# Performance work log

Measured on AMD Instinct MI355X. Metric: run time of the kernel, lower is better.

The kernel has to match this reference:

```python
import jax, jax.numpy as jnp
import numpy as np
from jax import lax

VEHICLE_LABELS = jnp.array([2, 3, 4, 6, 8], dtype=jnp.int64)
IMNET_MEAN = jnp.array([0.485, 0.456, 0.406], dtype=jnp.float32)
IMNET_STD = jnp.array([0.229, 0.224, 0.225], dtype=jnp.float32)
CROP = 64  # fixed RoIAlign output resolution replacing the variable-size python crop loop


def setup_inputs() -> dict:
    key = jax.random.key(0)
    ks = jax.random.split(key, 8)
    B, N, H, W = 8, 300, 512, 512
    x = jax.random.uniform(ks[0], (B, 3, H, W), dtype=jnp.float32)
    # well-formed boxes [x_min, y_min, x_max, y_max] inside the image
    tl = jax.random.uniform(ks[1], (B, N, 2), dtype=jnp.float32) * (W - 64.0)
    wh = jax.random.uniform(ks[2], (B, N, 2), dtype=jnp.float32) * 192.0 + 16.0
    br = jnp.minimum(tl + wh, float(W))
    boxes = jnp.concatenate([tl, br], axis=-1)  # [B,N,4]
    scores = jax.random.uniform(ks[3], (B, N), dtype=jnp.float32)
    labels = jax.random.randint(ks[4], (B, N), 0, 91).astype(jnp.int64)
    Wc = jax.random.normal(ks[5], (256, 3, 7, 7), dtype=jnp.float32) * 0.1
    bc = jnp.zeros((256,), dtype=jnp.float32)
    Wf = jax.random.normal(ks[6], (256, 4096), dtype=jnp.float32) / np.sqrt(256.0)
    bf = jnp.zeros((4096,), dtype=jnp.float32)
    return {"x": x, "boxes": boxes, "scores": scores, "labels": labels,
            "Wc": Wc, "bc": bc, "Wf": Wf, "bf": bf}


def extractor(imgs, Wc, bc, Wf, bf):
    # imgs [N,3,h,w] -> [N,4096]
    y = lax.conv_general_dilated(imgs, Wc, (4, 4), 'SAME',
                                 dimension_numbers=('NCHW', 'OIHW', 'NCHW'))
    y = jax.nn.relu(y + bc[None, :, None, None])
    y = y.mean(axis=(2, 3))  # global average pool -> [N,256]
    return y @ Wf + bf


def bilinear_sample(img, ys, xs):
    # img [C,H,W], ys [S], xs [S] -> [C,S,S]
    C, H, W = img.shape
    y0f = jnp.floor(ys); x0f = jnp.floor(xs)
    wy = (ys - y0f)[None, :, None]
    wx = (xs - x0f)[None, None, :]
    y0 = jnp.clip(y0f.astype(jnp.int32), 0, H - 1); y1 = jnp.clip(y0 + 1, 0, H - 1)
    x0 = jnp.clip(x0f.astype(jnp.int32), 0, W - 1); x1 = jnp.clip(x0 + 1, 0, W - 1)
    Ia = img[:, y0][:, :, x0]; Ib = img[:, y0][:, :, x1]
    Ic = img[:, y1][:, :, x0]; Id = img[:, y1][:, :, x1]
    return (Ia * (1 - wy) * (1 - wx) + Ib * (1 - wy) * wx
            + Ic * wy * (1 - wx) + Id * wy * wx)


def roi_align(img, box):
    # img [C,H,W], box [4] = x_min,y_min,x_max,y_max -> [C,CROP,CROP]
    t = (jnp.arange(CROP, dtype=img.dtype) + 0.5) / CROP
    ys = box[1] + t * (box[3] - box[1])
    xs = box[0] + t * (box[2] - box[0])
    return bilinear_sample(img, ys, xs)


def reference(x, boxes, scores, labels, Wc, bc, Wf, bf):
    score_threshold, K = 0.8, 20
    B = x.shape[0]
    # detection-weights transforms: ImageNet normalization
    images = (x - IMNET_MEAN[None, :, None, None]) / IMNET_STD[None, :, None, None]
    fullframe_features = extractor(images, Wc, bc, Wf, bf)  # [B,4096]
    # vehicle-class + score-threshold filtering, then top-k selection
    class_mask = (labels[..., None] == VEHICLE_LABELS[None, None, :]).any(-1)  # [B,N]
    comb_mask = class_mask & (scores > score_threshold)
    masked_scores = jnp.where(comb_mask, scores, -jnp.inf)
    vals, idx = lax.top_k(masked_scores, K)  # [B,K]
    valid = vals > -jnp.inf  # True where there is an object (matches torch code: 1=object)
    sel = jnp.take_along_axis(boxes, idx[..., None], axis=1)  # [B,K,4]
    Objects = jnp.where(valid[..., None], sel, 0.0)  # [B,K,4]
    # fused batched crop (RoIAlign) + batched extractor, replacing per-object loop
    crops = jax.vmap(lambda im, bxs: jax.vmap(lambda b: roi_align(im, b))(bxs))(images, Objects)  # [B,K,3,CROP,CROP]
    feats = extractor(crops.reshape(B * K, 3, CROP, CROP), Wc, bc, Wf, bf).reshape(B, K, 4096)
    degenerate = (Objects[..., 2] <= Objects[..., 0]) | (Objects[..., 3] <= Objects[..., 1])
    Object_features = jnp.where((valid & ~degenerate)[..., None], feats, 0.0)  # [B,K,4096]
    return Objects, Object_features, valid, fullframe_features
```

## Files before the change

kernel.cpp:

```cpp
#include <hip/hip_runtime.h>
#include <hip/hip_bf16.h>

#define OBJ_OFF   0
#define FEAT_OFF  640
#define VALID_OFF 656000
#define FF_OFF    656160

#define POOLED_N  (168 * 256)
#define SELBOX_N  (160 * 4)
#define FLAGS_N   (160)
#define K3        192

typedef __attribute__((ext_vector_type(8))) short short8v;
typedef __attribute__((ext_vector_type(4))) short short4v;
typedef __attribute__((ext_vector_type(4))) float f32x4;

__device__ __forceinline__ unsigned int rne_bf16(float f) {
    unsigned int u = __float_as_uint(f);
    return (u + 0x7FFFu + ((u >> 16) & 1u)) >> 16;
}

__global__ __launch_bounds__(256) void prep_kernel(
    const float* __restrict__ Wc, unsigned short* __restrict__ Wb,
    float* __restrict__ pooled)
{
    int i = blockIdx.x * 256 + threadIdx.x;
    if (i < POOLED_N) pooled[i] = 0.f;
    int oc = i / K3, k = i % K3;
    int c = k >> 6, r = (k >> 3) & 7, q = k & 7;
    float v = (r < 7 && q < 7) ? Wc[oc * 147 + c * 49 + r * 7 + q] : 0.f;
    Wb[i] = (unsigned short)rne_bf16(v);
}

__global__ __launch_bounds__(512) void topk_kernel(
    const float* __restrict__ boxes, const float* __restrict__ scores,
    const int* __restrict__ labels, float* __restrict__ d_out,
    float* __restrict__ selbox, float* __restrict__ flags)
{
    __shared__ unsigned long long keys[512];
    __shared__ unsigned long long red[512];
    const int b = blockIdx.x, t = threadIdx.x;

    unsigned long long key = 0ULL;
    if (t < 300) {
        float s = scores[b * 300 + t];
        int   l = labels[b * 300 + t];
        bool cls = (l == 2) || (l == 3) || (l == 4) || (l == 6) || (l == 8);
        if (cls && s > 0.8f) {
            key = ((unsigned long long)__float_as_uint(s) << 32) |
                  (unsigned long long)(unsigned int)(~(unsigned int)t);
        }
    }
    keys[t] = key;
    __syncthreads();

    for (int k = 0; k < 20; ++k) {
        red[t] = keys[t];
        __syncthreads();
        for (int s = 256; s > 0; s >>= 1) {
            if (t < s) red[t] = (red[t] > red[t + s]) ? red[t] : red[t + s];
            __syncthreads();
        }
        unsigned long long m = red[0];
        const int slot = b * 20 + k;
        if (m == 0ULL) {
            if (t == 0) {
                d_out[OBJ_OFF + slot * 4 + 0] = 0.f;
                d_out[OBJ_OFF + slot * 4 + 1] = 0.f;
                d_out[OBJ_OFF + slot * 4 + 2] = 0.f;
                d_out[OBJ_OFF + slot * 4 + 3] = 0.f;
                d_out[VALID_OFF + slot] = 0.f;
                selbox[slot * 4 + 0] = 0.f; selbox[slot * 4 + 1] = 0.f;
                selbox[slot * 4 + 2] = 0.f; selbox[slot * 4 + 3] = 0.f;
                flags[slot] = 0.f;
            }
        } else if (keys[t] == m) {
            const float bx0 = boxes[(b * 300 + t) * 4 + 0];
            const float by0 = boxes[(b * 300 + t) * 4 + 1];
            const float bx1 = boxes[(b * 300 + t) * 4 + 2];
            const float by1 = boxes[(b * 300 + t) * 4 + 3];
            d_out[OBJ_OFF + slot * 4 + 0] = bx0;
            d_out[OBJ_OFF + slot * 4 + 1] = by0;
            d_out[OBJ_OFF + slot * 4 + 2] = bx1;
            d_out[OBJ_OFF + slot * 4 + 3] = by1;
            d_out[VALID_OFF + slot] = 1.f;
            selbox[slot * 4 + 0] = bx0; selbox[slot * 4 + 1] = by0;
            selbox[slot * 4 + 2] = bx1; selbox[slot * 4 + 3] = by1;
            bool deg = (bx1 <= bx0) || (by1 <= by0);
            flags[slot] = deg ? 0.f : 1.f;
            keys[t] = 0ULL;
        }
        __syncthreads();
    }
}

__device__ __forceinline__ void conv_compute_regB(
    const unsigned short (&tb)[3][20][68], const short8v (&breg)[6][4],
    const float (&bias)[4], float (&poolacc)[4], int lr, int lq)
{
    f32x4 acc[4][4];
#pragma unroll
    for (int mf = 0; mf < 4; ++mf)
#pragma unroll
        for (int nf = 0; nf < 4; ++nf)
            acc[mf][nf] = (f32x4){0.f, 0.f, 0.f, 0.f};

#pragma unroll
    for (int ks = 0; ks < 6; ++ks) {
        const int kq = ks * 4 + lq;
        const int c = kq >> 3, rr = kq & 7;
        short8v a[4];
#pragma unroll
        for (int mf = 0; mf < 4; ++mf) {
            const unsigned short* ap = &tb[c][mf * 4 + rr][lr * 4];
            short4v a0 = *(const short4v*)ap;
            short4v a1 = *(const short4v*)(ap + 4);
            a[mf] = __builtin_shufflevector(a0, a1, 0, 1, 2, 3, 4, 5, 6, 7);
        }
#pragma unroll
        for (int mf = 0; mf < 4; ++mf)
#pragma unroll
            for (int nf = 0; nf < 4; ++nf)
                acc[mf][nf] = __builtin_amdgcn_mfma_f32_16x16x32_bf16(
                    a[mf], breg[ks][nf], acc[mf][nf], 0, 0, 0);
    }

#pragma unroll
    for (int nf = 0; nf < 4; ++nf) {
        float s = 0.f;
#pragma unroll
        for (int mf = 0; mf < 4; ++mf)
#pragma unroll
            for (int r = 0; r < 4; ++r) {
                float pv = acc[mf][nf][r] + bias[nf];
                s += pv > 0.f ? pv : 0.f;
            }
        poolacc[nf] += s;
    }
}

__device__ __forceinline__ void ff_stage_issue(
    const float* __restrict__ img, int iy0, int ix0, int tid, float (&sv)[16])
{
#pragma unroll
    for (int it = 0; it < 16; ++it) {
        int i = tid + it * 256;
        float v = 0.f;
        if (i < 4080) {
            int c = i / 1360, rem = i % 1360;
            int ir = rem / 68, icol = rem % 68;
            int gy = iy0 + ir, gx = ix0 + icol;
            if (gy >= 0 && gy < 512 && gx >= 0 && gx < 512)
                v = img[((size_t)c * 512 + gy) * 512 + gx];
        }
        sv[it] = v;
    }
}

__device__ __forceinline__ void ff_stage_write(
    unsigned short (&tb)[3][20][68], int iy0, int ix0, int tid,
    const float (&sv)[16], const float* mean, const float* istd)
{
#pragma unroll
    for (int it = 0; it < 16; ++it) {
        int i = tid + it * 256;
        if (i < 4080) {
            int c = i / 1360, rem = i % 1360;
            int ir = rem / 68, icol = rem % 68;
            int gy = iy0 + ir, gx = ix0 + icol;
            bool inb = (gy >= 0 && gy < 512 && gx >= 0 && gx < 512);
            float nv = inb ? (sv[it] - mean[c]) * istd[c] : 0.f;
            ((unsigned short*)tb)[i] = (unsigned short)rne_bf16(nv);
        }
    }
}

__global__ __launch_bounds__(256, 2) void ffconv_mfma(
    const float* __restrict__ x, const unsigned short* __restrict__ Wb,
    const float* __restrict__ bc, float* __restrict__ pooled)
{
    __shared__ __align__(16) unsigned short buf[2][3][20][68];
    const int b = blockIdx.y;
    const int tile_x = blockIdx.x & 7, rblk = blockIdx.x >> 3;
    const int tid = threadIdx.x;
    const int w = tid >> 6, l = tid & 63, lr = l & 15, lq = l >> 4;
    const int n0 = w * 64;
    const int ix0 = tile_x * 64 - 1;

    const float mean[3] = {0.485f, 0.456f, 0.406f};
    const float istd[3] = {1.0f / 0.229f, 1.0f / 0.224f, 1.0f / 0.225f};
    const float* __restrict__ img = x + (size_t)b * 3 * 512 * 512;

    short8v breg[6][4];
#pragma unroll
    for (int ks = 0; ks < 6; ++ks)
#pragma unroll
        for (int nf = 0; nf < 4; ++nf)
            breg[ks][nf] = *(const short8v*)&Wb[(size_t)(n0 + nf * 16 + lr) * K3 + ks * 32 + lq * 8];

    float bias[4];
#pragma unroll
    for (int nf = 0; nf < 4; ++nf) bias[nf] = bc[n0 + nf * 16 + lr];

    float poolacc[4] = {0.f, 0.f, 0.f, 0.f};
    float sv[16];

    ff_stage_issue(img, (rblk * 4 + 0) * 16 - 1, ix0, tid, sv);
    ff_stage_write(buf[0], (rblk * 4 + 0) * 16 - 1, ix0, tid, sv, mean, istd);
    __syncthreads();

#pragma unroll
    for (int q = 0; q < 4; ++q) {
        const int cur = q & 1;
        if (q < 3) ff_stage_issue(img, (rblk * 4 + q + 1) * 16 - 1, ix0, tid, sv);
        conv_compute_regB(buf[cur], breg, bias, poolacc, lr, lq);
        if (q < 3)
            ff_stage_write(buf[cur ^ 1], (rblk * 4 + q + 1) * 16 - 1, ix0, tid, sv, mean, istd);
        __syncthreads();
    }

#pragma unroll
    for (int nf = 0; nf < 4; ++nf) {
        float s = poolacc[nf];
        s += __shfl_down(s, 32);
        s += __shfl_down(s, 16);
        if (l < 16) atomicAdd(&pooled[b * 256 + n0 + nf * 16 + lr], s);
    }
}

__device__ __forceinline__ void conv_core(
    const unsigned short (&tile)[3][20][68],
    const unsigned short* __restrict__ Wb, const float* __restrict__ bc,
    float* __restrict__ pooled, int prow, int tid)
{
    const int w = tid >> 6, l = tid & 63;
    const int lr = l & 15, lq = l >> 4;
    const int n0 = w * 64;

    f32x4 acc[4][4];
#pragma unroll
    for (int mf = 0; mf < 4; ++mf)
#pragma unroll
        for (int nf = 0; nf < 4; ++nf)
            acc[mf][nf] = (f32x4){0.f, 0.f, 0.f, 0.f};

#pragma unroll
    for (int ks = 0; ks < 6; ++ks) {
        const int kq = ks * 4 + lq;
        const int c = kq >> 3, rr = kq & 7;
        const int koff = ks * 32 + lq * 8;

        short8v a[4], bfr[4];
#pragma unroll
        for (int mf = 0; mf < 4; ++mf) {
            const unsigned short* ap = &tile[c][mf * 4 + rr][lr * 4];
            short4v a0 = *(const short4v*)ap;
            short4v a1 = *(const short4v*)(ap + 4);
            a[mf] = __builtin_shufflevector(a0, a1, 0, 1, 2, 3, 4, 5, 6, 7);
        }
#pragma unroll
        for (int nf = 0; nf < 4; ++nf)
            bfr[nf] = *(const short8v*)&Wb[(size_t)(n0 + nf * 16 + lr) * K3 + koff];
#pragma unroll
        for (int mf = 0; mf < 4; ++mf)
#pragma unroll
            for (int nf = 0; nf < 4; ++nf)
                acc[mf][nf] = __builtin_amdgcn_mfma_f32_16x16x32_bf16(
                    a[mf], bfr[nf], acc[mf][nf], 0, 0, 0);
    }

#pragma unroll
    for (int nf = 0; nf < 4; ++nf) {
        const int oc = n0 + nf * 16 + lr;
        const float bias = bc[oc];
        float s = 0.f;
#pragma unroll
        for (int mf = 0; mf < 4; ++mf)
#pragma unroll
            for (int r = 0; r < 4; ++r) {
                float pv = acc[mf][nf][r] + bias;
                s += pv > 0.f ? pv : 0.f;
            }
        s += __shfl_down(s, 32);
        s += __shfl_down(s, 16);
        if (l < 16) atomicAdd(&pooled[prow * 256 + oc], s);
    }
}

__global__ __launch_bounds__(256, 2) void cropconv_mfma(
    const float* __restrict__ x, const unsigned short* __restrict__ Wb,
    const float* __restrict__ bc, const float* __restrict__ selbox,
    const float* __restrict__ flags, float* __restrict__ pooled)
{
    const int bk = blockIdx.x >> 2, quarter = blockIdx.x & 3;
    if (flags[bk] == 0.f) return;
    const int b = bk / 20;
    const int tid = threadIdx.x;

    __shared__ __align__(16) unsigned short tile[3][20][68];

    const float bx0 = selbox[bk * 4 + 0], by0 = selbox[bk * 4 + 1];
    const float bx1 = selbox[bk * 4 + 2], by1 = selbox[bk * 4 + 3];
    const float sy = (by1 - by0) * (1.f / 64.f);
    const float sx = (bx1 - bx0) * (1.f / 64.f);

    const float mean[3] = {0.485f, 0.456f, 0.406f};
    const float istd[3] = {1.0f / 0.229f, 1.0f / 0.224f, 1.0f / 0.225f};
    const float* __restrict__ img = x + (size_t)b * 3 * 512 * 512;

#pragma unroll
    for (int rd = 0; rd < 2; ++rd) {
        float rva[8], rvb[8], rvc[8], rvd[8], rwy[8], rwx[8];
#pragma unroll
        for (int e = 0; e < 8; ++e) {
            int i = tid + (rd * 8 + e) * 256;
            float Ia = 0.f, Ib = 0.f, Ic = 0.f, Id = 0.f, wy = 0.f, wx = 0.f;
            if (i < 4080) {
                int c = i / 1360, rem = i % 1360;
                int ir = rem / 68, icol = rem % 68;
                int cy = quarter * 16 - 1 + ir, cx = icol - 1;
                if (cy >= 0 && cy < 64 && cx >= 0 && cx < 64) {
                    float ys = by0 + ((float)cy + 0.5f) * sy;
                    float xs = bx0 + ((float)cx + 0.5f) * sx;
                    float yf = floorf(ys), xf = floorf(xs);
                    wy = ys - yf; wx = xs - xf;
                    int iy0 = min(max((int)yf, 0), 511), iy1 = min(iy0 + 1, 511);
                    int ix0 = min(max((int)xf, 0), 511), ix1 = min(ix0 + 1, 511);
                    const float* ch = img + (size_t)c * 512 * 512;
                    Ia = ch[iy0 * 512 + ix0]; Ib = ch[iy0 * 512 + ix1];
                    Ic = ch[iy1 * 512 + ix0]; Id = ch[iy1 * 512 + ix1];
                }
            }
            rva[e] = Ia; rvb[e] = Ib; rvc[e] = Ic; rvd[e] = Id;
            rwy[e] = wy; rwx[e] = wx;
        }
#pragma unroll
        for (int e = 0; e < 8; ++e) {
            int i = tid + (rd * 8 + e) * 256;
            if (i < 4080) {
                int c = i / 1360, rem = i % 1360;
                int ir = rem / 68, icol = rem % 68;
                int cy = quarter * 16 - 1 + ir, cx = icol - 1;
                float v = 0.f;
                if (cy >= 0 && cy < 64 && cx >= 0 && cx < 64) {
                    float wy = rwy[e], wx = rwx[e];
                    float s = rva[e] * (1.f - wy) * (1.f - wx) + rvb[e] * (1.f - wy) * wx +
                              rvc[e] * wy * (1.f - wx) + rvd[e] * wy * wx;
                    v = (s - mean[c]) * istd[c];
                }
                ((unsigned short*)tile)[i] = (unsigned short)rne_bf16(v);
            }
        }
    }
    __syncthreads();
    conv_core(tile, Wb, bc, pooled, 8 + bk, tid);
}

__global__ __launch_bounds__(256) void fc_kernel(
    const float* __restrict__ pooled, const float* __restrict__ Wf,
    const float* __restrict__ bf, const float* __restrict__ flags,
    float* __restrict__ d_out)
{
    __shared__ __align__(16) float p[24][64];
    const int cb = blockIdx.x, rg = blockIdx.y, kz = blockIdx.z;
    const int tid = threadIdx.x;

    for (int i = tid; i < 24 * 64; i += 256) {
        int r = i >> 6, k = i & 63;
        int R = rg * 24 + r;
        float s = (R < 8) ? (1.f / 16384.f) : (1.f / 256.f);
        p[r][k] = pooled[R * 256 + kz * 64 + k] * s;
    }
    __syncthreads();

    float acc[24];
#pragma unroll
    for (int r = 0; r < 24; ++r) acc[r] = 0.f;

    const int col = cb * 256 + tid;
    const float* wp = Wf + (size_t)(kz * 64) * 4096 + col;
    for (int k = 0; k < 64; k += 4) {
        float w0 = wp[(size_t)(k + 0) * 4096];
        float w1 = wp[(size_t)(k + 1) * 4096];
        float w2 = wp[(size_t)(k + 2) * 4096];
        float w3 = wp[(size_t)(k + 3) * 4096];
#pragma unroll
        for (int r = 0; r < 24; ++r) {
            float4 pv = *(const float4*)&p[r][k];
            acc[r] += pv.x * w0 + pv.y * w1 + pv.z * w2 + pv.w * w3;
        }
    }

    const float bias_on = (kz == 0) ? 1.f : 0.f;
#pragma unroll
    for (int r = 0; r < 24; ++r) {
        int R = rg * 24 + r;
        float v = acc[r] + bias_on * bf[col];
        if (R < 8) {
            atomicAdd(&d_out[FF_OFF + R * 4096 + col], v);
        } else {
            int rr = R - 8;
            if (flags[rr] != 0.f)
                atomicAdd(&d_out[FEAT_OFF + rr * 4096 + col], v);
        }
    }
}

extern "C" void kernel_launch(void* const* d_in, const int* in_sizes, int n_in,
                              void* d_out, int out_size, void* d_ws, size_t ws_size,
                              hipStream_t stream)
{
    const float* x      = (const float*)d_in[0];
    const float* boxes  = (const float*)d_in[1];
    const float* scores = (const float*)d_in[2];
    const int*   labels = (const int*)d_in[3];
    const float* Wc     = (const float*)d_in[4];
    const float* bc     = (const float*)d_in[5];
    const float* Wf     = (const float*)d_in[6];
    const float* bf     = (const float*)d_in[7];
    float* out = (float*)d_out;

    float* pooled = (float*)d_ws;
    float* selbox = pooled + POOLED_N;
    float* flags  = selbox + SELBOX_N;
    unsigned short* Wb = (unsigned short*)(flags + FLAGS_N);

    hipMemsetAsync(d_out, 0, (size_t)out_size * sizeof(float), stream);

    prep_kernel<<<K3, 256, 0, stream>>>(Wc, Wb, pooled);
    topk_kernel<<<8, 512, 0, stream>>>(boxes, scores, labels, out, selbox, flags);
    ffconv_mfma<<<dim3(64, 8), 256, 0, stream>>>(x, Wb, bc, pooled);
    cropconv_mfma<<<640, 256, 0, stream>>>(x, Wb, bc, selbox, flags, pooled);
    fc_kernel<<<dim3(16, 7, 4), 256, 0, stream>>>(pooled, Wf, bf, flags, out);
}
```

Baseline: 228.3 us.

## Load conv weights per k-step, drop min-occupancy bounds, halve FC row groups

The full-frame conv no longer preloads all 24 weight fragments into registers. It now reloads them from global memory at each k-step through a shared conv_compute helper that the crop conv also uses. The launch_bounds minimum-blocks hint of 2 is removed from both conv kernels. The FC kernel processes 12 rows per block instead of 24, doubling the grid in y. The aim is lower register pressure and more parallelism in the FC kernel, at the cost of repeated weight loads and more atomics and blocks.

```diff
diff --git a/kernel.cpp b/kernel.cpp
--- a/kernel.cpp
+++ b/kernel.cpp
@@ -94,9 +94,10 @@
     }
 }
 
-__device__ __forceinline__ void conv_compute_regB(
-    const unsigned short (&tb)[3][20][68], const short8v (&breg)[6][4],
-    const float (&bias)[4], float (&poolacc)[4], int lr, int lq)
+__device__ __forceinline__ void conv_compute(
+    const unsigned short (&tb)[3][20][68],
+    const unsigned short* __restrict__ Wb, const float (&bias)[4],
+    float (&poolacc)[4], int n0, int lr, int lq)
 {
     f32x4 acc[4][4];
 #pragma unroll
@@ -109,7 +110,12 @@
     for (int ks = 0; ks < 6; ++ks) {
         const int kq = ks * 4 + lq;
         const int c = kq >> 3, rr = kq & 7;
-        short8v a[4];
+        const int koff = ks * 32 + lq * 8;
+
+        short8v a[4], bfr[4];
+#pragma unroll
+        for (int nf = 0; nf < 4; ++nf)
+            bfr[nf] = *(const short8v*)&Wb[(size_t)(n0 + nf * 16 + lr) * K3 + koff];
 #pragma unroll
         for (int mf = 0; mf < 4; ++mf) {
             const unsigned short* ap = &tb[c][mf * 4 + rr][lr * 4];
@@ -122,7 +128,7 @@
 #pragma unroll
             for (int nf = 0; nf < 4; ++nf)
                 acc[mf][nf] = __builtin_amdgcn_mfma_f32_16x16x32_bf16(
-                    a[mf], breg[ks][nf], acc[mf][nf], 0, 0, 0);
+                    a[mf], bfr[nf], acc[mf][nf], 0, 0, 0);
     }
 
 #pragma unroll
@@ -175,7 +181,7 @@
     }
 }
 
-__global__ __launch_bounds__(256, 2) void ffconv_mfma(
+__global__ __launch_bounds__(256) void ffconv_mfma(
     const float* __restrict__ x, const unsigned short* __restrict__ Wb,
     const float* __restrict__ bc, float* __restrict__ pooled)
 {
@@ -191,13 +197,6 @@
     const float istd[3] = {1.0f / 0.229f, 1.0f / 0.224f, 1.0f / 0.225f};
     const float* __restrict__ img = x + (size_t)b * 3 * 512 * 512;
 
-    short8v breg[6][4];
-#pragma unroll
-    for (int ks = 0; ks < 6; ++ks)
-#pragma unroll
-        for (int nf = 0; nf < 4; ++nf)
-            breg[ks][nf] = *(const short8v*)&Wb[(size_t)(n0 + nf * 16 + lr) * K3 + ks * 32 + lq * 8];
-
     float bias[4];
 #pragma unroll
     for (int nf = 0; nf < 4; ++nf) bias[nf] = bc[n0 + nf * 16 + lr];
@@ -213,7 +212,7 @@
     for (int q = 0; q < 4; ++q) {
         const int cur = q & 1;
         if (q < 3) ff_stage_issue(img, (rblk * 4 + q + 1) * 16 - 1, ix0, tid, sv);
-        conv_compute_regB(buf[cur], breg, bias, poolacc, lr, lq);
+        conv_compute(buf[cur], Wb, bias, poolacc, n0, lr, lq);
         if (q < 3)
             ff_stage_write(buf[cur ^ 1], (rblk * 4 + q + 1) * 16 - 1, ix0, tid, sv, mean, istd);
         __syncthreads();
@@ -228,66 +227,7 @@
     }
 }
 
-__device__ __forceinline__ void conv_core(
-    const unsigned short (&tile)[3][20][68],
-    const unsigned short* __restrict__ Wb, const float* __restrict__ bc,
-    float* __restrict__ pooled, int prow, int tid)
-{
-    const int w = tid >> 6, l = tid & 63;
-    const int lr = l & 15, lq = l >> 4;
-    const int n0 = w * 64;
-
-    f32x4 acc[4][4];
-#pragma unroll
-    for (int mf = 0; mf < 4; ++mf)
-#pragma unroll
-        for (int nf = 0; nf < 4; ++nf)
-            acc[mf][nf] = (f32x4){0.f, 0.f, 0.f, 0.f};
-
-#pragma unroll
-    for (int ks = 0; ks < 6; ++ks) {
-        const int kq = ks * 4 + lq;
-        const int c = kq >> 3, rr = kq & 7;
-        const int koff = ks * 32 + lq * 8;
-
-        short8v a[4], bfr[4];
-#pragma unroll
-        for (int mf = 0; mf < 4; ++mf) {
-            const unsigned short* ap = &tile[c][mf * 4 + rr][lr * 4];
-            short4v a0 = *(const short4v*)ap;
-            short4v a1 = *(const short4v*)(ap + 4);
-            a[mf] = __builtin_shufflevector(a0, a1, 0, 1, 2, 3, 4, 5, 6, 7);
-        }
-#pragma unroll
-        for (int nf = 0; nf < 4; ++nf)
-            bfr[nf] = *(const short8v*)&Wb[(size_t)(n0 + nf * 16 + lr) * K3 + koff];
-#pragma unroll
-        for (int mf = 0; mf < 4; ++mf)
-#pragma unroll
-            for (int nf = 0; nf < 4; ++nf)
-                acc[mf][nf] = __builtin_amdgcn_mfma_f32_16x16x32_bf16(
-                    a[mf], bfr[nf], acc[mf][nf], 0, 0, 0);
-    }
-
-#pragma unroll
-    for (int nf = 0; nf < 4; ++nf) {
-        const int oc = n0 + nf * 16 + lr;
-        const float bias = bc[oc];
-        float s = 0.f;
-#pragma unroll
-        for (int mf = 0; mf < 4; ++mf)
-#pragma unroll
-            for (int r = 0; r < 4; ++r) {
-                float pv = acc[mf][nf][r] + bias;
-                s += pv > 0.f ? pv : 0.f;
-            }
-        s += __shfl_down(s, 32);
-        s += __shfl_down(s, 16);
-        if (l < 16) atomicAdd(&pooled[prow * 256 + oc], s);
-    }
-}
-
-__global__ __launch_bounds__(256, 2) void cropconv_mfma(
+__global__ __launch_bounds__(256) void cropconv_mfma(
     const float* __restrict__ x, const unsigned short* __restrict__ Wb,
     const float* __restrict__ bc, const float* __restrict__ selbox,
     const float* __restrict__ flags, float* __restrict__ pooled)
@@ -353,7 +293,23 @@
         }
     }
     __syncthreads();
-    conv_core(tile, Wb, bc, pooled, 8 + bk, tid);
+
+    const int w = tid >> 6, l = tid & 63, lr = l & 15, lq = l >> 4;
+    const int n0 = w * 64;
+    float bias[4];
+#pragma unroll
+    for (int nf = 0; nf < 4; ++nf) bias[nf] = bc[n0 + nf * 16 + lr];
+    float poolacc[4] = {0.f, 0.f, 0.f, 0.f};
+
+    conv_compute(tile, Wb, bias, poolacc, n0, lr, lq);
+
+#pragma unroll
+    for (int nf = 0; nf < 4; ++nf) {
+        float s = poolacc[nf];
+        s += __shfl_down(s, 32);
+        s += __shfl_down(s, 16);
+        if (l < 16) atomicAdd(&pooled[(8 + bk) * 256 + n0 + nf * 16 + lr], s);
+    }
 }
 
 __global__ __launch_bounds__(256) void fc_kernel(
@@ -361,21 +317,21 @@
     const float* __restrict__ bf, const float* __restrict__ flags,
     float* __restrict__ d_out)
 {
-    __shared__ __align__(16) float p[24][64];
+    __shared__ __align__(16) float p[12][64];
     const int cb = blockIdx.x, rg = blockIdx.y, kz = blockIdx.z;
     const int tid = threadIdx.x;
 
-    for (int i = tid; i < 24 * 64; i += 256) {
+    for (int i = tid; i < 12 * 64; i += 256) {
         int r = i >> 6, k = i & 63;
-        int R = rg * 24 + r;
+        int R = rg * 12 + r;
         float s = (R < 8) ? (1.f / 16384.f) : (1.f / 256.f);
         p[r][k] = pooled[R * 256 + kz * 64 + k] * s;
     }
     __syncthreads();
 
-    float acc[24];
-#pragma unroll
-    for (int r = 0; r < 24; ++r) acc[r] = 0.f;
+    float acc[12];
+#pragma unroll
+    for (int r = 0; r < 12; ++r) acc[r] = 0.f;
 
     const int col = cb * 256 + tid;
     const float* wp = Wf + (size_t)(kz * 64) * 4096 + col;
@@ -385,7 +341,7 @@
         float w2 = wp[(size_t)(k + 2) * 4096];
         float w3 = wp[(size_t)(k + 3) * 4096];
 #pragma unroll
-        for (int r = 0; r < 24; ++r) {
+        for (int r = 0; r < 12; ++r) {
             float4 pv = *(const float4*)&p[r][k];
             acc[r] += pv.x * w0 + pv.y * w1 + pv.z * w2 + pv.w * w3;
         }
@@ -393,8 +349,8 @@
 
     const float bias_on = (kz == 0) ? 1.f : 0.f;
 #pragma unroll
-    for (int r = 0; r < 24; ++r) {
-        int R = rg * 24 + r;
+    for (int r = 0; r < 12; ++r) {
+        int R = rg * 12 + r;
         float v = acc[r] + bias_on * bf[col];
         if (R < 8) {
             atomicAdd(&d_out[FF_OFF + R * 4096 + col], v);
@@ -431,5 +387,5 @@
     topk_kernel<<<8, 512, 0, stream>>>(boxes, scores, labels, out, selbox, flags);
     ffconv_mfma<<<dim3(64, 8), 256, 0, stream>>>(x, Wb, bc, pooled);
     cropconv_mfma<<<640, 256, 0, stream>>>(x, Wb, bc, selbox, flags, pooled);
-    fc_kernel<<<dim3(16, 7, 4), 256, 0, stream>>>(pooled, Wf, bf, flags, out);
-}
+    fc_kernel<<<dim3(16, 14, 4), 256, 0, stream>>>(pooled, Wf, bf, flags, out);
+}
```

Measured after the change: 185.0 us. 18.9% less time.
